# Kernel tuning notes

Measured on AMD Instinct MI355X. Metric: run time of the kernel, lower is better.

Reference implementation:

```python
import jax, jax.numpy as jnp
import numpy as np

R, B, TAU, SINKHORN_ITERS = 64, 16, 0.5, 5
D_MODEL = 1024
BATCH = 2048


def setup_inputs() -> dict:
    key = jax.random.key(0)
    k1, k2, k3, k4, k5 = jax.random.split(key, 5)
    return {
        "x_t": jax.random.normal(k1, (BATCH, D_MODEL), dtype=jnp.float32),
        "h": jax.random.normal(k2, (BATCH, R * B), dtype=jnp.float32),
        "W_perm": jax.random.normal(k3, (D_MODEL, R * B * B), dtype=jnp.float32) * 0.02,
        "W_diag": jax.random.normal(k4, (D_MODEL, R * B), dtype=jnp.float32) * 0.02,
        "W_alpha": jax.random.normal(k5, (D_MODEL, R * B), dtype=jnp.float32) * 0.02,
    }


def _sinkhorn(log_alpha):
    # 5 iterations of alternating row/col log-normalization
    def body(la, _):
        la = la - jax.nn.logsumexp(la, axis=-1, keepdims=True)
        la = la - jax.nn.logsumexp(la, axis=-2, keepdims=True)
        return la, None
    la, _ = jax.lax.scan(body, log_alpha, None, length=SINKHORN_ITERS)
    return jnp.exp(la)


def reference(x_t, h, W_perm, W_diag, W_alpha):
    batch = x_t.shape[0]
    # (batch, r, b, b) log-space assignment logits
    logits = (x_t @ W_perm).reshape(batch, R, B, B) / TAU
    soft_perm = _sinkhorn(logits)
    # straight-through hard permutation: argmax over rows (dim=-2) per column
    idx = jnp.argmax(soft_perm, axis=-2)                      # (batch, r, b)
    hard = jax.nn.one_hot(idx, B, axis=-2, dtype=soft_perm.dtype)  # (batch, r, b, b)
    perm = jax.lax.stop_gradient(hard - soft_perm) + soft_perm
    h_blocks = h.reshape(batch, R, B)
    h_permuted = jnp.einsum('brij,brj->bri', perm, h_blocks)
    alpha = jax.nn.sigmoid((x_t @ W_alpha)).reshape(batch, R, B)
    diag_vals = alpha * jnp.tanh((x_t @ W_diag).reshape(batch, R, B))
    return (diag_vals * h_permuted).reshape(batch, R * B)
```

## Files before the change

kernel.cpp:

```cpp
#include <hip/hip_runtime.h>


#define D_MODEL 1024
#define RDIM 64
#define BDIM 16
#define NBATCH 2048
#define MB 64
#define XS_LD 68

#define XSZ 2097152
#define WPSZ 16777216
#define WDSZ 1048576

#define OFF_XS   0u
#define OFF_WPS  12582912u
#define OFF_WDS  113246208u
#define OFF_WAS  117440512u
#define WS_NEED  121634816u

#define LSCALE 2.8853900817779268f

typedef __attribute__((ext_vector_type(8))) short short8;
typedef __attribute__((ext_vector_type(4))) float f32x4;
#define MFMA_BF16 __builtin_amdgcn_mfma_f32_16x16x32_bf16

__device__ __forceinline__ unsigned short f2bf_rne(float f) {
    unsigned u = __float_as_uint(f);
    unsigned r = (u + 0x7fffu + ((u >> 16) & 1u)) >> 16;
    return (unsigned short)r;
}
__device__ __forceinline__ float bf2f(unsigned short s) {
    return __uint_as_float(((unsigned)s) << 16);
}

__global__ void k_split_x(const float* __restrict__ x, unsigned short* __restrict__ XS) {
    const int i = blockIdx.x * 256 + threadIdx.x;
    const float v = x[i];
    const unsigned short s1 = f2bf_rne(v);
    const float r1 = v - bf2f(s1);
    const unsigned short s2 = f2bf_rne(r1);
    const float r2 = r1 - bf2f(s2);
    XS[i] = s1; XS[XSZ + i] = s2; XS[2 * XSZ + i] = f2bf_rne(r2);
}

__global__ void k_split_w(const float* __restrict__ W, unsigned short* __restrict__ dst) {
    __shared__ float tile[32][65];
    const int t = threadIdx.x;
    const int c0 = blockIdx.x * 64;
    const int kt = blockIdx.y;
    #pragma unroll
    for (int i = 0; i < 8; i++) {
        const int k = (t >> 6) * 8 + i;
        tile[k][t & 63] = W[(long)(kt * 32 + k) * 16384 + c0 + (t & 63)];
    }
    __syncthreads();
    #pragma unroll
    for (int i = 0; i < 8; i++) {
        const int cl = (t >> 5) * 8 + i;
        const int c = c0 + cl;
        const int rr = c >> 8, nn = c & 255;
        const int k = t & 31;
        const float v = tile[k][cl];
        const long off = (((long)(rr * 32 + kt) * 256) + nn) * 32 + k;
        const unsigned short s1 = f2bf_rne(v);
        const float r1 = v - bf2f(s1);
        const unsigned short s2 = f2bf_rne(r1);
        const float r2 = r1 - bf2f(s2);
        dst[off] = s1;
        dst[WPSZ + off] = s2;
        dst[2 * (long)WPSZ + off] = f2bf_rne(r2);
    }
}

__global__ void k_split_w2(const float* __restrict__ Wd, const float* __restrict__ Wa,
                           unsigned short* __restrict__ WDS_, unsigned short* __restrict__ WAS_) {
    __shared__ float tile[32][65];
    const float* W = blockIdx.z ? Wa : Wd;
    unsigned short* dst = blockIdx.z ? WAS_ : WDS_;
    const int t = threadIdx.x;
    const int c0 = blockIdx.x * 64;
    const int kt = blockIdx.y;
    #pragma unroll
    for (int i = 0; i < 8; i++) {
        const int k = (t >> 6) * 8 + i;
        tile[k][t & 63] = W[(long)(kt * 32 + k) * 1024 + c0 + (t & 63)];
    }
    __syncthreads();
    #pragma unroll
    for (int i = 0; i < 8; i++) {
        const int cl = (t >> 5) * 8 + i;
        const int c = c0 + cl;
        const int rr = c >> 4, nn = c & 15;
        const int k = t & 31;
        const float v = tile[k][cl];
        const int off = ((rr * 32 + kt) * 16 + nn) * 32 + k;
        const unsigned short s1 = f2bf_rne(v);
        const float r1 = v - bf2f(s1);
        dst[off] = s1;
        dst[WDSZ + off] = f2bf_rne(r1);
    }
}

__global__ __launch_bounds__(256, 3)
void bmf_mfma_kernel(const unsigned short* __restrict__ XS,
                     const unsigned short* __restrict__ WPS,
                     const unsigned short* __restrict__ WDS,
                     const unsigned short* __restrict__ WAS,
                     const float* __restrict__ h,
                     float* __restrict__ out)
{
    __shared__ __align__(16) float sm[12800];
    float* la   = sm;
    float* dval = sm + 8704;
    float* aval = dval + 1024;
    float* hv   = aval + 1024;
    float* hpm  = hv + 1024;

    const int t   = threadIdx.x;
    const int l   = t & 63;
    const int w   = t >> 6;
    const int bid = blockIdx.x;
    const int r   = ((bid >> 8) << 3) | (bid & 7);
    const int bt  = (bid >> 3) & 31;
    const int b0  = bt * MB;
    const int quad = l >> 4, l15 = l & 15;

    f32x4 acc[4][4];
    f32x4 acc2[2];
    #pragma unroll
    for (int a = 0; a < 4; a++)
        #pragma unroll
        for (int b = 0; b < 4; b++) acc[a][b] = (f32x4){0.f, 0.f, 0.f, 0.f};
    acc2[0] = (f32x4){0.f, 0.f, 0.f, 0.f};
    acc2[1] = (f32x4){0.f, 0.f, 0.f, 0.f};

    const int isAlpha = w >> 1;
    const int mtPair  = w & 1;
    const unsigned short* WX = isAlpha ? WAS : WDS;

    const unsigned short* aB0 = XS + (b0 + l15) * 1024 + quad * 8;
    const unsigned short* aB1 = aB0 + XSZ;
    const unsigned short* aB2 = aB1 + XSZ;
    const unsigned short* bB0 = WPS + r * 262144 + ((w * 4) * 16 + l15) * 32 + quad * 8;
    const unsigned short* bB1 = bB0 + WPSZ;
    const unsigned short* bB2 = bB1 + WPSZ;
    const unsigned short* wB0 = WX + r * 16384 + l15 * 32 + quad * 8;
    const unsigned short* wB1 = wB0 + WDSZ;

    for (int ks = 0; ks < 32; ++ks) {
        const int bo = ks * 8192;
        short8 bf0[4], bf1[4], bf2[4];
        #pragma unroll
        for (int ntl = 0; ntl < 4; ntl++) {
            bf0[ntl] = *(const short8*)(bB0 + bo + ntl * 512);
            bf1[ntl] = *(const short8*)(bB1 + bo + ntl * 512);
            bf2[ntl] = *(const short8*)(bB2 + bo + ntl * 512);
        }
        const short8 wf0 = *(const short8*)(wB0 + ks * 512);
        const short8 wf1 = *(const short8*)(wB1 + ks * 512);
        const int ao = ks * 32;
        #pragma unroll
        for (int mt = 0; mt < 4; mt++) {
            const short8 a0 = *(const short8*)(aB0 + mt * 16384 + ao);
            const short8 a1 = *(const short8*)(aB1 + mt * 16384 + ao);
            const short8 a2 = *(const short8*)(aB2 + mt * 16384 + ao);
            #pragma unroll
            for (int ntl = 0; ntl < 4; ntl++) {
                f32x4 c = acc[mt][ntl];
                c = MFMA_BF16(a0, bf0[ntl], c, 0, 0, 0);
                c = MFMA_BF16(a0, bf1[ntl], c, 0, 0, 0);
                c = MFMA_BF16(a1, bf0[ntl], c, 0, 0, 0);
                c = MFMA_BF16(a0, bf2[ntl], c, 0, 0, 0);
                c = MFMA_BF16(a1, bf1[ntl], c, 0, 0, 0);
                c = MFMA_BF16(a2, bf0[ntl], c, 0, 0, 0);
                acc[mt][ntl] = c;
            }
            if ((mt >> 1) == mtPair) {
                const int mi = mt & 1;
                f32x4 c2 = acc2[mi];
                c2 = MFMA_BF16(a0, wf0, c2, 0, 0, 0);
                c2 = MFMA_BF16(a0, wf1, c2, 0, 0, 0);
                c2 = MFMA_BF16(a1, wf0, c2, 0, 0, 0);
                acc2[mi] = c2;
            }
        }
    }

    {
        float* arr = isAlpha ? aval : dval;
        #pragma unroll
        for (int mi = 0; mi < 2; mi++) {
            #pragma unroll
            for (int q = 0; q < 4; q++) {
                const int row = (mtPair * 2 + mi) * 16 + quad * 4 + q;
                arr[row * 16 + l15] = acc2[mi][q];
            }
        }
    }
    #pragma unroll
    for (int q = 0; q < 4; q++) {
        const int id  = t + 256 * q;
        const int row = id >> 4, j = id & 15;
        hv[id]  = h[(long)(b0 + row) * D_MODEL + r * BDIM + j];
        hpm[id] = 0.f;
    }
    __syncthreads();

    for (int half = 0; half < 2; ++half) {
        #pragma unroll
        for (int mi = 0; mi < 2; mi++) {
            const int mt = half * 2 + mi;
            #pragma unroll
            for (int ntl = 0; ntl < 4; ntl++) {
                #pragma unroll
                for (int q = 0; q < 4; q++) {
                    const int ml = mi * 16 + quad * 4 + q;
                    la[ml * 272 + (w * 4 + ntl) * 17 + l15] = acc[mt][ntl][q] * LSCALE;
                }
            }
        }
        __syncthreads();

        for (int it = 0; it < 5; ++it) {
            #pragma unroll
            for (int q = 0; q < 2; q++) {
                const int id = t + 256 * q;
                const int m = id >> 4, i = id & 15;
                float* rowp = la + m * 272 + i * 17;
                float mx = rowp[0];
                #pragma unroll
                for (int j = 1; j < 16; j++) mx = fmaxf(mx, rowp[j]);
                float s = 0.f;
                #pragma unroll
                for (int j = 0; j < 16; j++) s += exp2f(rowp[j] - mx);
                const float lse = mx + log2f(s);
                #pragma unroll
                for (int j = 0; j < 16; j++) rowp[j] -= lse;
            }
            __syncthreads();
            #pragma unroll
            for (int q = 0; q < 2; q++) {
                const int id = t + 256 * q;
                const int m = id >> 4, j = id & 15;
                float* colp = la + m * 272 + j;
                float mx = colp[0];
                #pragma unroll
                for (int i = 1; i < 16; i++) mx = fmaxf(mx, colp[i * 17]);
                float s = 0.f;
                #pragma unroll
                for (int i = 0; i < 16; i++) s += exp2f(colp[i * 17] - mx);
                const float lse = mx + log2f(s);
                #pragma unroll
                for (int i = 0; i < 16; i++) colp[i * 17] -= lse;
            }
            __syncthreads();
        }
        #pragma unroll
        for (int q = 0; q < 2; q++) {
            const int id = t + 256 * q;
            const int m = id >> 4, j = id & 15;
            const float* colp = la + m * 272 + j;
            float best = colp[0]; int bi = 0;
            #pragma unroll
            for (int i = 1; i < 16; i++) {
                const float v = colp[i * 17];
                if (v > best) { best = v; bi = i; }
            }
            const int gm = half * 32 + m;
            atomicAdd(&hpm[gm * 16 + bi], hv[gm * 16 + j]);
        }
        __syncthreads();
    }

    #pragma unroll
    for (int q = 0; q < 4; q++) {
        const int id  = t + 256 * q;
        const int row = id >> 4, i = id & 15;
        const float A  = aval[id];
        const float Dv = dval[id];
        const float sg = 1.0f / (1.0f + expf(-A));
        out[(long)(b0 + row) * D_MODEL + r * BDIM + i] = sg * tanhf(Dv) * hpm[id];
    }
}

__global__ __launch_bounds__(256, 2)
void bmf_fused_kernel(const float* __restrict__ x,
                      const float* __restrict__ h,
                      const float* __restrict__ Wp,
                      const float* __restrict__ Wd,
                      const float* __restrict__ Wa,
                      float* __restrict__ out)
{
    __shared__ float sm[15488];
    float* xs   = sm;
    float* wsh  = sm + 32 * XS_LD;
    float* w2s  = wsh + 32 * 256;
    float* la   = sm;
    float* dval = sm + 11392;
    float* aval = dval + 1024;
    float* hv   = aval + 1024;
    float* hpm  = hv + 1024;

    const int t   = threadIdx.x;
    const int bid = blockIdx.x;
    const int r   = bid >> 5;
    const int b0  = (bid & 31) * MB;
    const long rcol0 = (long)r * (BDIM * BDIM);

    const int tr  = t >> 5;
    const int tc  = t & 31;
    const int cAi = tc * 4;
    const int cBi = 128 + tc * 4;
    const int row2 = t >> 2;
    const int c2   = (t & 3) * 8;

    float acc[8][8];
    float acc2[8];
    #pragma unroll
    for (int i = 0; i < 8; i++) {
        acc2[i] = 0.f;
        #pragma unroll
        for (int j = 0; j < 8; j++) acc[i][j] = 0.f;
    }

    for (int ks = 0; ks < D_MODEL / 32; ++ks) {
        const int k0 = ks * 32;
        {
            const int row = t >> 2, kq = t & 3;
            #pragma unroll
            for (int e = 0; e < 2; e++) {
                const int kk = kq * 4 + e * 16;
                const float4 g = *(const float4*)(x + (long)(b0 + row) * D_MODEL + k0 + kk);
                xs[(kk + 0) * XS_LD + row] = g.x;
                xs[(kk + 1) * XS_LD + row] = g.y;
                xs[(kk + 2) * XS_LD + row] = g.z;
                xs[(kk + 3) * XS_LD + row] = g.w;
            }
        }
        {
            const int rbase = t >> 6;
            const int colf  = (t & 63) * 4;
            #pragma unroll
            for (int rep = 0; rep < 8; rep++) {
                const int rowk = rbase + rep * 4;
                const float4 g = *(const float4*)(Wp + (long)(k0 + rowk) * (RDIM * BDIM * BDIM) + rcol0 + colf);
                *(float4*)(wsh + rowk * 256 + colf) = g;
            }
        }
        {
            const int kr = t >> 3;
            const int c  = (t & 7) * 4;
            const float* src = (c < 16)
                ? (Wd + (long)(k0 + kr) * D_MODEL + r * BDIM + c)
                : (Wa + (long)(k0 + kr) * D_MODEL + r * BDIM + (c - 16));
            const float4 g = *(const float4*)src;
            *(float4*)(w2s + kr * 32 + c) = g;
        }
        __syncthreads();
        #pragma unroll
        for (int kk = 0; kk < 32; ++kk) {
            const float4 xlo = *(const float4*)(xs + kk * XS_LD + tr * 8);
            const float4 xhi = *(const float4*)(xs + kk * XS_LD + tr * 8 + 4);
            const float4 wA  = *(const float4*)(wsh + kk * 256 + cAi);
            const float4 wB  = *(const float4*)(wsh + kk * 256 + cBi);
            const float xv[8] = {xlo.x, xlo.y, xlo.z, xlo.w, xhi.x, xhi.y, xhi.z, xhi.w};
            #pragma unroll
            for (int ri = 0; ri < 8; ri++) {
                acc[ri][0] += xv[ri] * wA.x; acc[ri][1] += xv[ri] * wA.y;
                acc[ri][2] += xv[ri] * wA.z; acc[ri][3] += xv[ri] * wA.w;
                acc[ri][4] += xv[ri] * wB.x; acc[ri][5] += xv[ri] * wB.y;
                acc[ri][6] += xv[ri] * wB.z; acc[ri][7] += xv[ri] * wB.w;
            }
            const float xv2 = xs[kk * XS_LD + row2];
            const float4 u0 = *(const float4*)(w2s + kk * 32 + c2);
            const float4 u1 = *(const float4*)(w2s + kk * 32 + c2 + 4);
            acc2[0] += xv2 * u0.x; acc2[1] += xv2 * u0.y;
            acc2[2] += xv2 * u0.z; acc2[3] += xv2 * u0.w;
            acc2[4] += xv2 * u1.x; acc2[5] += xv2 * u1.y;
            acc2[6] += xv2 * u1.z; acc2[7] += xv2 * u1.w;
        }
        __syncthreads();
    }

    #pragma unroll
    for (int e = 0; e < 8; e++) {
        const int c = c2 + e;
        if (c < 16) dval[row2 * 16 + c] = acc2[e];
        else        aval[row2 * 16 + (c - 16)] = acc2[e];
    }
    #pragma unroll
    for (int q = 0; q < 4; q++) {
        const int id  = t + 256 * q;
        const int row = id >> 4, j = id & 15;
        hv[id]  = h[(long)(b0 + row) * D_MODEL + r * BDIM + j];
        hpm[id] = 0.f;
    }
    __syncthreads();

    for (int half = 0; half < 2; ++half) {
        if ((tr >> 2) == half) {
            const int mbase = (tr & 3) * 8;
            #pragma unroll
            for (int ri = 0; ri < 8; ri++) {
                const int m = mbase + ri;
                #pragma unroll
                for (int e = 0; e < 8; e++) {
                    const int col = (e < 4) ? (cAi + e) : (cBi + e - 4);
                    la[m * 272 + (col >> 4) * 17 + (col & 15)] = acc[ri][e] * 2.0f;
                }
            }
        }
        __syncthreads();

        for (int it = 0; it < 5; ++it) {
            #pragma unroll
            for (int q = 0; q < 2; q++) {
                const int id = t + 256 * q;
                const int m = id >> 4, i = id & 15;
                float* rowp = la + m * 272 + i * 17;
                float mx = rowp[0];
                #pragma unroll
                for (int j = 1; j < 16; j++) mx = fmaxf(mx, rowp[j]);
                float s = 0.f;
                #pragma unroll
                for (int j = 0; j < 16; j++) s += expf(rowp[j] - mx);
                const float lse = mx + logf(s);
                #pragma unroll
                for (int j = 0; j < 16; j++) rowp[j] -= lse;
            }
            __syncthreads();
            #pragma unroll
            for (int q = 0; q < 2; q++) {
                const int id = t + 256 * q;
                const int m = id >> 4, j = id & 15;
                float* colp = la + m * 272 + j;
                float mx = colp[0];
                #pragma unroll
                for (int i = 1; i < 16; i++) mx = fmaxf(mx, colp[i * 17]);
                float s = 0.f;
                #pragma unroll
                for (int i = 0; i < 16; i++) s += expf(colp[i * 17] - mx);
                const float lse = mx + logf(s);
                #pragma unroll
                for (int i = 0; i < 16; i++) colp[i * 17] -= lse;
            }
            __syncthreads();
        }
        #pragma unroll
        for (int q = 0; q < 2; q++) {
            const int id = t + 256 * q;
            const int m = id >> 4, j = id & 15;
            const float* colp = la + m * 272 + j;
            float best = colp[0]; int bi = 0;
            #pragma unroll
            for (int i = 1; i < 16; i++) {
                const float v = colp[i * 17];
                if (v > best) { best = v; bi = i; }
            }
            const int gm = half * 32 + m;
            atomicAdd(&hpm[gm * 16 + bi], hv[gm * 16 + j]);
        }
        __syncthreads();
    }

    #pragma unroll
    for (int q = 0; q < 4; q++) {
        const int id  = t + 256 * q;
        const int row = id >> 4, i = id & 15;
        const float A  = aval[id];
        const float Dv = dval[id];
        const float sg = 1.0f / (1.0f + expf(-A));
        out[(long)(b0 + row) * D_MODEL + r * BDIM + i] = sg * tanhf(Dv) * hpm[id];
    }
}

extern "C" void kernel_launch(void* const* d_in, const int* in_sizes, int n_in,
                              void* d_out, int out_size, void* d_ws, size_t ws_size,
                              hipStream_t stream) {
    const float* x  = (const float*)d_in[0];
    const float* h  = (const float*)d_in[1];
    const float* Wp = (const float*)d_in[2];
    const float* Wd = (const float*)d_in[3];
    const float* Wa = (const float*)d_in[4];
    float* out = (float*)d_out;

    if (ws_size >= (size_t)WS_NEED) {
        unsigned short* XS  = (unsigned short*)((char*)d_ws + OFF_XS);
        unsigned short* WPS = (unsigned short*)((char*)d_ws + OFF_WPS);
        unsigned short* WDS = (unsigned short*)((char*)d_ws + OFF_WDS);
        unsigned short* WAS = (unsigned short*)((char*)d_ws + OFF_WAS);
        k_split_x<<<dim3(XSZ / 256), dim3(256), 0, stream>>>(x, XS);
        k_split_w<<<dim3(256, 32), dim3(256), 0, stream>>>(Wp, WPS);
        k_split_w2<<<dim3(16, 32, 2), dim3(256), 0, stream>>>(Wd, Wa, WDS, WAS);
        bmf_mfma_kernel<<<dim3(2048), dim3(256), 0, stream>>>(XS, WPS, WDS, WAS, h, out);
    } else {
        bmf_fused_kernel<<<dim3(2048), dim3(256), 0, stream>>>(x, h, Wp, Wd, Wa, out);
    }
}
```

Baseline: 733.8 us.

## Stage X tiles in LDS via direct loads, double M-tile, vectorize split kernels

The main MFMA kernel now processes 128 batch rows per block instead of 64, halving the grid. The three bf16 splits of X are staged into shared memory with global_load_lds, and all four waves reuse them. This halves redundant reads of the large W_perm split per output and removes per-wave global loads of X. The split-preprocessing kernels also move to float4 loads and short8 stores. The cost is more accumulator registers, with occupancy dropped to 2 blocks per SM, plus larger LDS use and two barriers per K chunk.

Result: slower. 1.115 ms (+52.0%).

```diff
diff --git a/kernel.cpp b/kernel.cpp
--- a/kernel.cpp
+++ b/kernel.cpp
@@ -3,10 +3,7 @@
 
 #define D_MODEL 1024
 #define RDIM 64
-#define BDIM 16
 #define NBATCH 2048
-#define MB 64
-#define XS_LD 68
 
 #define XSZ 2097152
 #define WPSZ 16777216
@@ -24,6 +21,10 @@
 typedef __attribute__((ext_vector_type(4))) float f32x4;
 #define MFMA_BF16 __builtin_amdgcn_mfma_f32_16x16x32_bf16
 
+#define GLOAD_LDS16(g, lp) __builtin_amdgcn_global_load_lds( \
+    (const __attribute__((address_space(1))) unsigned int*)(g), \
+    (__attribute__((address_space(3))) unsigned int*)(lp), 16, 0, 0)
+
 __device__ __forceinline__ unsigned short f2bf_rne(float f) {
     unsigned u = __float_as_uint(f);
     unsigned r = (u + 0x7fffu + ((u >> 16) & 1u)) >> 16;
@@ -34,74 +35,87 @@
 }
 
 __global__ void k_split_x(const float* __restrict__ x, unsigned short* __restrict__ XS) {
-    const int i = blockIdx.x * 256 + threadIdx.x;
-    const float v = x[i];
-    const unsigned short s1 = f2bf_rne(v);
-    const float r1 = v - bf2f(s1);
-    const unsigned short s2 = f2bf_rne(r1);
-    const float r2 = r1 - bf2f(s2);
-    XS[i] = s1; XS[XSZ + i] = s2; XS[2 * XSZ + i] = f2bf_rne(r2);
+    const int i = (blockIdx.x * 256 + threadIdx.x) * 4;
+    const float4 v = *(const float4*)(x + i);
+    const float vv[4] = {v.x, v.y, v.z, v.w};
+    unsigned short p1[4], p2[4], p3[4];
+    #pragma unroll
+    for (int e = 0; e < 4; e++) {
+        const unsigned short s1 = f2bf_rne(vv[e]);
+        const float r1 = vv[e] - bf2f(s1);
+        const unsigned short s2 = f2bf_rne(r1);
+        p1[e] = s1; p2[e] = s2; p3[e] = f2bf_rne(r1 - bf2f(s2));
+    }
+    #pragma unroll
+    for (int e = 0; e < 4; e++) {
+        XS[i + e] = p1[e];
+        XS[XSZ + i + e] = p2[e];
+        XS[2 * XSZ + i + e] = p3[e];
+    }
 }
 
 __global__ void k_split_w(const float* __restrict__ W, unsigned short* __restrict__ dst) {
-    __shared__ float tile[32][65];
+    __shared__ float tile[32][72];
     const int t = threadIdx.x;
     const int c0 = blockIdx.x * 64;
     const int kt = blockIdx.y;
-    #pragma unroll
-    for (int i = 0; i < 8; i++) {
-        const int k = (t >> 6) * 8 + i;
-        tile[k][t & 63] = W[(long)(kt * 32 + k) * 16384 + c0 + (t & 63)];
+    {
+        const int kr = t >> 3, cq = (t & 7) * 8;
+        const float* src = W + (long)(kt * 32 + kr) * 16384 + c0 + cq;
+        *(float4*)&tile[kr][cq]     = *(const float4*)src;
+        *(float4*)&tile[kr][cq + 4] = *(const float4*)(src + 4);
     }
     __syncthreads();
-    #pragma unroll
-    for (int i = 0; i < 8; i++) {
-        const int cl = (t >> 5) * 8 + i;
-        const int c = c0 + cl;
-        const int rr = c >> 8, nn = c & 255;
-        const int k = t & 31;
-        const float v = tile[k][cl];
-        const long off = (((long)(rr * 32 + kt) * 256) + nn) * 32 + k;
+    const int kq = t & 3, cl = t >> 2;
+    const int c = c0 + cl;
+    const int rr = c >> 8, nn = c & 255;
+    short8 o1, o2, o3;
+    #pragma unroll
+    for (int j = 0; j < 8; j++) {
+        const float v = tile[kq * 8 + j][cl];
         const unsigned short s1 = f2bf_rne(v);
         const float r1 = v - bf2f(s1);
         const unsigned short s2 = f2bf_rne(r1);
-        const float r2 = r1 - bf2f(s2);
-        dst[off] = s1;
-        dst[WPSZ + off] = s2;
-        dst[2 * (long)WPSZ + off] = f2bf_rne(r2);
-    }
+        o1[j] = (short)s1; o2[j] = (short)s2; o3[j] = (short)f2bf_rne(r1 - bf2f(s2));
+    }
+    const long off = (((long)(rr * 32 + kt) * 256) + nn) * 32 + kq * 8;
+    *(short8*)(dst + off) = o1;
+    *(short8*)(dst + WPSZ + off) = o2;
+    *(short8*)(dst + 2 * (long)WPSZ + off) = o3;
 }
 
 __global__ void k_split_w2(const float* __restrict__ Wd, const float* __restrict__ Wa,
                            unsigned short* __restrict__ WDS_, unsigned short* __restrict__ WAS_) {
-    __shared__ float tile[32][65];
+    __shared__ float tile[32][72];
     const float* W = blockIdx.z ? Wa : Wd;
     unsigned short* dst = blockIdx.z ? WAS_ : WDS_;
     const int t = threadIdx.x;
     const int c0 = blockIdx.x * 64;
     const int kt = blockIdx.y;
-    #pragma unroll
-    for (int i = 0; i < 8; i++) {
-        const int k = (t >> 6) * 8 + i;
-        tile[k][t & 63] = W[(long)(kt * 32 + k) * 1024 + c0 + (t & 63)];
+    {
+        const int kr = t >> 3, cq = (t & 7) * 8;
+        const float* src = W + (long)(kt * 32 + kr) * 1024 + c0 + cq;
+        *(float4*)&tile[kr][cq]     = *(const float4*)src;
+        *(float4*)&tile[kr][cq + 4] = *(const float4*)(src + 4);
     }
     __syncthreads();
-    #pragma unroll
-    for (int i = 0; i < 8; i++) {
-        const int cl = (t >> 5) * 8 + i;
-        const int c = c0 + cl;
-        const int rr = c >> 4, nn = c & 15;
-        const int k = t & 31;
-        const float v = tile[k][cl];
-        const int off = ((rr * 32 + kt) * 16 + nn) * 32 + k;
+    const int kq = t & 3, cl = t >> 2;
+    const int c = c0 + cl;
+    const int rr = c >> 4, nn = c & 15;
+    short8 o1, o2;
+    #pragma unroll
+    for (int j = 0; j < 8; j++) {
+        const float v = tile[kq * 8 + j][cl];
         const unsigned short s1 = f2bf_rne(v);
-        const float r1 = v - bf2f(s1);
-        dst[off] = s1;
-        dst[WDSZ + off] = f2bf_rne(r1);
-    }
-}
-
-__global__ __launch_bounds__(256, 3)
+        o1[j] = (short)s1;
+        o2[j] = (short)f2bf_rne(v - bf2f(s1));
+    }
+    const int off = ((rr * 32 + kt) * 16 + nn) * 32 + kq * 8;
+    *(short8*)(dst + off) = o1;
+    *(short8*)(dst + WDSZ + off) = o2;
+}
+
+__global__ __launch_bounds__(256, 2)
 void bmf_mfma_kernel(const unsigned short* __restrict__ XS,
                      const unsigned short* __restrict__ WPS,
                      const unsigned short* __restrict__ WDS,
@@ -109,113 +123,125 @@
                      const float* __restrict__ h,
                      float* __restrict__ out)
 {
-    __shared__ __align__(16) float sm[12800];
+    __shared__ __align__(16) float sm[16896];
+    char* smc   = (char*)sm;
     float* la   = sm;
     float* dval = sm + 8704;
-    float* aval = dval + 1024;
-    float* hv   = aval + 1024;
-    float* hpm  = hv + 1024;
-
-    const int t   = threadIdx.x;
-    const int l   = t & 63;
-    const int w   = t >> 6;
+    float* aval = dval + 2048;
+    float* hv   = aval + 2048;
+    float* hpm  = hv + 2048;
+
+    const int t = threadIdx.x;
+    const int l = t & 63;
+    const int w = t >> 6;
     const int bid = blockIdx.x;
-    const int r   = ((bid >> 8) << 3) | (bid & 7);
-    const int bt  = (bid >> 3) & 31;
-    const int b0  = bt * MB;
+    const int r  = ((bid >> 7) << 3) | (bid & 7);
+    const int bt = (bid >> 3) & 15;
+    const int b0 = bt * 128;
     const int quad = l >> 4, l15 = l & 15;
 
-    f32x4 acc[4][4];
-    f32x4 acc2[2];
-    #pragma unroll
-    for (int a = 0; a < 4; a++)
+    f32x4 acc[8][4];
+    f32x4 acc2[4];
+    #pragma unroll
+    for (int a = 0; a < 8; a++)
         #pragma unroll
         for (int b = 0; b < 4; b++) acc[a][b] = (f32x4){0.f, 0.f, 0.f, 0.f};
-    acc2[0] = (f32x4){0.f, 0.f, 0.f, 0.f};
-    acc2[1] = (f32x4){0.f, 0.f, 0.f, 0.f};
+    #pragma unroll
+    for (int a = 0; a < 4; a++) acc2[a] = (f32x4){0.f, 0.f, 0.f, 0.f};
 
     const int isAlpha = w >> 1;
-    const int mtPair  = w & 1;
+    const int rowHalf = w & 1;
     const unsigned short* WX = isAlpha ? WAS : WDS;
 
-    const unsigned short* aB0 = XS + (b0 + l15) * 1024 + quad * 8;
-    const unsigned short* aB1 = aB0 + XSZ;
-    const unsigned short* aB2 = aB1 + XSZ;
-    const unsigned short* bB0 = WPS + r * 262144 + ((w * 4) * 16 + l15) * 32 + quad * 8;
-    const unsigned short* bB1 = bB0 + WPSZ;
-    const unsigned short* bB2 = bB1 + WPSZ;
-    const unsigned short* wB0 = WX + r * 16384 + l15 * 32 + quad * 8;
-    const unsigned short* wB1 = wB0 + WDSZ;
-
-    for (int ks = 0; ks < 32; ++ks) {
-        const int bo = ks * 8192;
-        short8 bf0[4], bf1[4], bf2[4];
-        #pragma unroll
-        for (int ntl = 0; ntl < 4; ntl++) {
-            bf0[ntl] = *(const short8*)(bB0 + bo + ntl * 512);
-            bf1[ntl] = *(const short8*)(bB1 + bo + ntl * 512);
-            bf2[ntl] = *(const short8*)(bB2 + bo + ntl * 512);
-        }
-        const short8 wf0 = *(const short8*)(wB0 + ks * 512);
-        const short8 wf1 = *(const short8*)(wB1 + ks * 512);
-        const int ao = ks * 32;
-        #pragma unroll
-        for (int mt = 0; mt < 4; mt++) {
-            const short8 a0 = *(const short8*)(aB0 + mt * 16384 + ao);
-            const short8 a1 = *(const short8*)(aB1 + mt * 16384 + ao);
-            const short8 a2 = *(const short8*)(aB2 + mt * 16384 + ao);
-            #pragma unroll
-            for (int ntl = 0; ntl < 4; ntl++) {
-                f32x4 c = acc[mt][ntl];
-                c = MFMA_BF16(a0, bf0[ntl], c, 0, 0, 0);
-                c = MFMA_BF16(a0, bf1[ntl], c, 0, 0, 0);
-                c = MFMA_BF16(a1, bf0[ntl], c, 0, 0, 0);
-                c = MFMA_BF16(a0, bf2[ntl], c, 0, 0, 0);
-                c = MFMA_BF16(a1, bf1[ntl], c, 0, 0, 0);
-                c = MFMA_BF16(a2, bf0[ntl], c, 0, 0, 0);
-                acc[mt][ntl] = c;
-            }
-            if ((mt >> 1) == mtPair) {
-                const int mi = mt & 1;
-                f32x4 c2 = acc2[mi];
-                c2 = MFMA_BF16(a0, wf0, c2, 0, 0, 0);
-                c2 = MFMA_BF16(a0, wf1, c2, 0, 0, 0);
-                c2 = MFMA_BF16(a1, wf0, c2, 0, 0, 0);
-                acc2[mi] = c2;
-            }
-        }
+    const unsigned short* bP = WPS + r * 262144 + ((w * 4) * 16 + l15) * 32 + quad * 8;
+    const unsigned short* wP = WX + r * 16384 + l15 * 32 + quad * 8;
+
+    for (int kc = 0; kc < 16; ++kc) {
+        #pragma unroll
+        for (int s = 0; s < 12; ++s) {
+            const int slot = w * 12 + s;
+            const int hf = slot & 1;
+            const int reg = slot >> 1;
+            const int q_ = reg & 3;
+            const int ps = reg >> 2;
+            const unsigned short* g = XS + (ps >> 1) * XSZ
+                + (b0 + hf * 64 + l) * 1024 + kc * 64 + (ps & 1) * 32 + q_ * 8;
+            GLOAD_LDS16(g, smc + slot * 1024);
+        }
+        __syncthreads();
+        #pragma unroll
+        for (int sb = 0; sb < 2; ++sb) {
+            const int ks = kc * 2 + sb;
+            const unsigned short* bS = bP + ks * 8192;
+            short8 bf0[4], bf1[4], bf2[4];
+            #pragma unroll
+            for (int n = 0; n < 4; n++) {
+                bf0[n] = *(const short8*)(bS + n * 512);
+                bf1[n] = *(const short8*)(bS + n * 512 + WPSZ);
+                bf2[n] = *(const short8*)(bS + n * 512 + 2 * (long)WPSZ);
+            }
+            const short8 wf0 = *(const short8*)(wP + ks * 512);
+            const short8 wf1 = *(const short8*)(wP + ks * 512 + WDSZ);
+            #pragma unroll
+            for (int mt = 0; mt < 8; mt++) {
+                const int ro = (mt * 16 + l15) * 16;
+                const short8 a0 = *(const short8*)(smc + ((0 * 2 + sb) * 4 + quad) * 2048 + ro);
+                const short8 a1 = *(const short8*)(smc + ((1 * 2 + sb) * 4 + quad) * 2048 + ro);
+                const short8 a2 = *(const short8*)(smc + ((2 * 2 + sb) * 4 + quad) * 2048 + ro);
+                #pragma unroll
+                for (int n = 0; n < 4; n++) {
+                    f32x4 c = acc[mt][n];
+                    c = MFMA_BF16(a0, bf0[n], c, 0, 0, 0);
+                    c = MFMA_BF16(a0, bf1[n], c, 0, 0, 0);
+                    c = MFMA_BF16(a1, bf0[n], c, 0, 0, 0);
+                    c = MFMA_BF16(a0, bf2[n], c, 0, 0, 0);
+                    c = MFMA_BF16(a1, bf1[n], c, 0, 0, 0);
+                    c = MFMA_BF16(a2, bf0[n], c, 0, 0, 0);
+                    acc[mt][n] = c;
+                }
+                if ((mt >> 2) == rowHalf) {
+                    const int mi = mt & 3;
+                    f32x4 c2 = acc2[mi];
+                    c2 = MFMA_BF16(a0, wf0, c2, 0, 0, 0);
+                    c2 = MFMA_BF16(a0, wf1, c2, 0, 0, 0);
+                    c2 = MFMA_BF16(a1, wf0, c2, 0, 0, 0);
+                    acc2[mi] = c2;
+                }
+            }
+        }
+        __syncthreads();
     }
 
     {
         float* arr = isAlpha ? aval : dval;
         #pragma unroll
-        for (int mi = 0; mi < 2; mi++) {
+        for (int mi = 0; mi < 4; mi++) {
             #pragma unroll
             for (int q = 0; q < 4; q++) {
-                const int row = (mtPair * 2 + mi) * 16 + quad * 4 + q;
+                const int row = (rowHalf * 4 + mi) * 16 + quad * 4 + q;
                 arr[row * 16 + l15] = acc2[mi][q];
             }
         }
     }
     #pragma unroll
-    for (int q = 0; q < 4; q++) {
+    for (int q = 0; q < 8; q++) {
         const int id  = t + 256 * q;
         const int row = id >> 4, j = id & 15;
-        hv[id]  = h[(long)(b0 + row) * D_MODEL + r * BDIM + j];
+        hv[id]  = h[(long)(b0 + row) * D_MODEL + r * 16 + j];
         hpm[id] = 0.f;
     }
     __syncthreads();
 
-    for (int half = 0; half < 2; ++half) {
+    for (int ch = 0; ch < 4; ++ch) {
         #pragma unroll
         for (int mi = 0; mi < 2; mi++) {
-            const int mt = half * 2 + mi;
-            #pragma unroll
-            for (int ntl = 0; ntl < 4; ntl++) {
+            const int mt = ch * 2 + mi;
+            #pragma unroll
+            for (int n = 0; n < 4; n++) {
                 #pragma unroll
                 for (int q = 0; q < 4; q++) {
                     const int ml = mi * 16 + quad * 4 + q;
-                    la[ml * 272 + (w * 4 + ntl) * 17 + l15] = acc[mt][ntl][q] * LSCALE;
+                    la[ml * 272 + (w * 4 + n) * 17 + l15] = acc[mt][n][q] * LSCALE;
                 }
             }
         }
@@ -266,20 +292,20 @@
                 const float v = colp[i * 17];
                 if (v > best) { best = v; bi = i; }
             }
-            const int gm = half * 32 + m;
+            const int gm = ch * 32 + m;
             atomicAdd(&hpm[gm * 16 + bi], hv[gm * 16 + j]);
         }
         __syncthreads();
     }
 
     #pragma unroll
-    for (int q = 0; q < 4; q++) {
+    for (int q = 0; q < 8; q++) {
         const int id  = t + 256 * q;
         const int row = id >> 4, i = id & 15;
         const float A  = aval[id];
         const float Dv = dval[id];
         const float sg = 1.0f / (1.0f + expf(-A));
-        out[(long)(b0 + row) * D_MODEL + r * BDIM + i] = sg * tanhf(Dv) * hpm[id];
+        out[(long)(b0 + row) * D_MODEL + r * 16 + i] = sg * tanhf(Dv) * hpm[id];
     }
 }
 
@@ -293,7 +319,7 @@
 {
     __shared__ float sm[15488];
     float* xs   = sm;
-    float* wsh  = sm + 32 * XS_LD;
+    float* wsh  = sm + 32 * 68;
     float* w2s  = wsh + 32 * 256;
     float* la   = sm;
     float* dval = sm + 11392;
@@ -304,8 +330,8 @@
     const int t   = threadIdx.x;
     const int bid = blockIdx.x;
     const int r   = bid >> 5;
-    const int b0  = (bid & 31) * MB;
-    const long rcol0 = (long)r * (BDIM * BDIM);
+    const int b0  = (bid & 31) * 64;
+    const long rcol0 = (long)r * 256;
 
     const int tr  = t >> 5;
     const int tc  = t & 31;
@@ -323,18 +349,18 @@
         for (int j = 0; j < 8; j++) acc[i][j] = 0.f;
     }
 
-    for (int ks = 0; ks < D_MODEL / 32; ++ks) {
+    for (int ks = 0; ks < 32; ++ks) {
         const int k0 = ks * 32;
         {
             const int row = t >> 2, kq = t & 3;
             #pragma unroll
             for (int e = 0; e < 2; e++) {
                 const int kk = kq * 4 + e * 16;
-                const float4 g = *(const float4*)(x + (long)(b0 + row) * D_MODEL + k0 + kk);
-                xs[(kk + 0) * XS_LD + row] = g.x;
-                xs[(kk + 1) * XS_LD + row] = g.y;
-                xs[(kk + 2) * XS_LD + row] = g.z;
-                xs[(kk + 3) * XS_LD + row] = g.w;
+                const float4 g = *(const float4*)(x + (long)(b0 + row) * 1024 + k0 + kk);
+                xs[(kk + 0) * 68 + row] = g.x;
+                xs[(kk + 1) * 68 + row] = g.y;
+                xs[(kk + 2) * 68 + row] = g.z;
+                xs[(kk + 3) * 68 + row] = g.w;
             }
         }
         {
@@ -343,7 +369,7 @@
             #pragma unroll
             for (int rep = 0; rep < 8; rep++) {
                 const int rowk = rbase + rep * 4;
-                const float4 g = *(const float4*)(Wp + (long)(k0 + rowk) * (RDIM * BDIM * BDIM) + rcol0 + colf);
+                const float4 g = *(const float4*)(Wp + (long)(k0 + rowk) * 16384 + rcol0 + colf);
                 *(float4*)(wsh + rowk * 256 + colf) = g;
             }
         }
@@ -351,16 +377,16 @@
             const int kr = t >> 3;
             const int c  = (t & 7) * 4;
             const float* src = (c < 16)
-                ? (Wd + (long)(k0 + kr) * D_MODEL + r * BDIM + c)
-                : (Wa + (long)(k0 + kr) * D_MODEL + r * BDIM + (c - 16));
+                ? (Wd + (long)(k0 + kr) * 1024 + r * 16 + c)
+                : (Wa + (long)(k0 + kr) * 1024 + r * 16 + (c - 16));
             const float4 g = *(const float4*)src;
             *(float4*)(w2s + kr * 32 + c) = g;
         }
         __syncthreads();
         #pragma unroll
         for (int kk = 0; kk < 32; ++kk) {
-            const float4 xlo = *(const float4*)(xs + kk * XS_LD + tr * 8);
-            const float4 xhi = *(const float4*)(xs + kk * XS_LD + tr * 8 + 4);
+            const float4 xlo = *(const float4*)(xs + kk * 68 + tr * 8);
+            const float4 xhi = *(const float4*)(xs + kk * 68 + tr * 8 + 4);
             const float4 wA  = *(const float4*)(wsh + kk * 256 + cAi);
             const float4 wB  = *(const float4*)(wsh + kk * 256 + cBi);
             const float xv[8] = {xlo.x, xlo.y, xlo.z, xlo.w, xhi.x, xhi.y, xhi.z, xhi.w};
@@ -371,7 +397,7 @@
                 acc[ri][4] += xv[ri] * wB.x; acc[ri][5] += xv[ri] * wB.y;
                 acc[ri][6] += xv[ri] * wB.z; acc[ri][7] += xv[ri] * wB.w;
             }
-            const float xv2 = xs[kk * XS_LD + row2];
+            const float xv2 = xs[kk * 68 + row2];
             const float4 u0 = *(const float4*)(w2s + kk * 32 + c2);
             const float4 u1 = *(const float4*)(w2s + kk * 32 + c2 + 4);
             acc2[0] += xv2 * u0.x; acc2[1] += xv2 * u0.y;
@@ -392,7 +418,7 @@
     for (int q = 0; q < 4; q++) {
         const int id  = t + 256 * q;
         const int row = id >> 4, j = id & 15;
-        hv[id]  = h[(long)(b0 + row) * D_MODEL + r * BDIM + j];
+        hv[id]  = h[(long)(b0 + row) * 1024 + r * 16 + j];
         hpm[id] = 0.f;
     }
     __syncthreads();
@@ -470,7 +496,7 @@
         const float A  = aval[id];
         const float Dv = dval[id];
         const float sg = 1.0f / (1.0f + expf(-A));
-        out[(long)(b0 + row) * D_MODEL + r * BDIM + i] = sg * tanhf(Dv) * hpm[id];
+        out[(long)(b0 + row) * 1024 + r * 16 + i] = sg * tanhf(Dv) * hpm[id];
     }
 }
 
@@ -489,10 +515,10 @@
         unsigned short* WPS = (unsigned short*)((char*)d_ws + OFF_WPS);
         unsigned short* WDS = (unsigned short*)((char*)d_ws + OFF_WDS);
         unsigned short* WAS = (unsigned short*)((char*)d_ws + OFF_WAS);
-        k_split_x<<<dim3(XSZ / 256), dim3(256), 0, stream>>>(x, XS);
+        k_split_x<<<dim3(XSZ / 1024), dim3(256), 0, stream>>>(x, XS);
         k_split_w<<<dim3(256, 32), dim3(256), 0, stream>>>(Wp, WPS);
         k_split_w2<<<dim3(16, 32, 2), dim3(256), 0, stream>>>(Wd, Wa, WDS, WAS);
-        bmf_mfma_kernel<<<dim3(2048), dim3(256), 0, stream>>>(XS, WPS, WDS, WAS, h, out);
+        bmf_mfma_kernel<<<dim3(1024), dim3(256), 0, stream>>>(XS, WPS, WDS, WAS, h, out);
     } else {
         bmf_fused_kernel<<<dim3(2048), dim3(256), 0, stream>>>(x, h, Wp, Wd, Wa, out);
     }
```
